# Kernel optimization log

Measured on AMD Instinct MI355X. Metric: run time of the kernel, lower is better.

## Reference

```python
import jax, jax.numpy as jnp
import numpy as np

V, B, C, H, W, D = 3, 2, 16, 128, 128, 32


def _skew(w):
    wx, wy, wz = w[..., 0], w[..., 1], w[..., 2]
    z = jnp.zeros_like(wx)
    return jnp.stack([
        jnp.stack([z, -wz, wy], -1),
        jnp.stack([wz, z, -wx], -1),
        jnp.stack([-wy, wx, z], -1)], -2)


def _rodrigues(w):
    th = jnp.linalg.norm(w, axis=-1, keepdims=True)
    n = w / (th + 1e-8)
    K = _skew(n)
    th = th[..., None]
    I = jnp.eye(3, dtype=w.dtype)
    return I + jnp.sin(th) * K + (1.0 - jnp.cos(th)) * (K @ K)


def setup_inputs() -> dict:
    key = jax.random.key(0)
    k1, k2, k3, k4 = jax.random.split(key, 4)
    features = jax.random.normal(k1, (V, B, C, H, W), jnp.float32)
    Kmat = jnp.array([[1.2 * W, 0.0, W / 2.0], [0.0, 1.2 * W, H / 2.0], [0.0, 0.0, 1.0]], jnp.float32)
    intrinsics = jnp.tile(Kmat, (V, B, 1, 1))
    rotvec = 0.05 * jax.random.normal(k2, (V, B, 3), jnp.float32)
    R = _rodrigues(rotvec)                                  # (V,B,3,3)
    t = 0.1 * jax.random.normal(k3, (V, B, 3), jnp.float32)
    top = jnp.concatenate([R, t[..., None]], -1)            # (V,B,3,4)
    bot = jnp.broadcast_to(jnp.array([0.0, 0.0, 0.0, 1.0], jnp.float32), (V, B, 1, 4))
    cam_to_world = jnp.concatenate([top, bot], -2)          # (V,B,4,4)
    depth_hypo = 1.0 + 9.0 * jax.random.uniform(k4, (B, D, H, W), jnp.float32)
    return {"features": features, "intrinsics": intrinsics,
            "cam_to_world": cam_to_world, "depth_hypo": depth_hypo}


def _grid_sample(img, grid):
    # img (B,C,H,W), grid (B,Hg,Wg,2) in [-1,1]; bilinear, zeros padding, align_corners=False
    Bb, Cc, Hh, Ww = img.shape
    gx = (grid[..., 0] + 1.0) * (Ww * 0.5) - 0.5
    gy = (grid[..., 1] + 1.0) * (Hh * 0.5) - 0.5
    x0f, y0f = jnp.floor(gx), jnp.floor(gy)
    fx, fy = gx - x0f, gy - y0f
    x0, y0 = x0f.astype(jnp.int32), y0f.astype(jnp.int32)

    def gather(xi, yi):
        valid = ((xi >= 0) & (xi < Ww) & (yi >= 0) & (yi < Hh)).astype(img.dtype)
        xc = jnp.clip(xi, 0, Ww - 1)
        yc = jnp.clip(yi, 0, Hh - 1)
        v = jax.vmap(lambda im, y, x: im[:, y, x])(img, yc, xc)  # (B,C,Hg,Wg)
        return v * valid[:, None]

    v00 = gather(x0, y0)
    v01 = gather(x0 + 1, y0)
    v10 = gather(x0, y0 + 1)
    v11 = gather(x0 + 1, y0 + 1)
    fx_, fy_ = fx[:, None], fy[:, None]
    return (v00 * (1 - fx_) * (1 - fy_) + v01 * fx_ * (1 - fy_)
            + v10 * (1 - fx_) * fy_ + v11 * fx_ * fy_)


def _unfold5(x):
    # x (B,K,H,W) -> (B,K,25,H,W); kernel 5, stride 1, pad 2; row-major kernel order (torch F.unfold)
    Hh, Ww = x.shape[-2], x.shape[-1]
    xp = jnp.pad(x, ((0, 0), (0, 0), (2, 2), (2, 2)))
    return jnp.stack([xp[..., i:i + Hh, j:j + Ww] for i in range(5) for j in range(5)], axis=2)


def _safe_norm(x, axis, keepdims=False):
    s = jnp.sum(x * x, axis=axis, keepdims=keepdims)
    z = s == 0
    return jnp.where(z, 0.0, jnp.sqrt(jnp.where(z, 1.0, s)))


def _homo_warp(src_f, depth_hypo, src_K, src_c2w, ref_K, ref_c2w):
    Bb, Cc, Hh, Ww = src_f.shape
    Dd = depth_hypo.shape[1]
    src_w2c = jnp.linalg.inv(src_c2w)
    ref_w2c = jnp.linalg.inv(ref_c2w)
    src_KK = src_w2c.at[:, :3, :3].set(src_K)
    ref_KK = ref_w2c.at[:, :3, :3].set(ref_K)
    proj = (src_KK @ src_w2c) @ jnp.linalg.inv(ref_KK @ ref_w2c)
    rot, trans = proj[:, :3, :3], proj[:, :3, 3:4]
    # NOTE: source uses arange(height) for both axes (square images assumed)
    ys, xs = jnp.meshgrid(jnp.arange(Hh, dtype=jnp.float32), jnp.arange(Hh, dtype=jnp.float32), indexing='ij')
    xyz = jnp.stack([xs.ravel(), ys.ravel(), jnp.ones(Hh * Ww, jnp.float32)], 0)  # (3,HW)
    rot_xyz = jnp.einsum('bij,jn->bin', rot, xyz)                                 # (B,3,HW)
    pts = rot_xyz[:, :, None, :] * depth_hypo.reshape(Bb, 1, Dd, -1) + trans[:, :, None, :]
    xy = pts[:, :2] / pts[:, 2:3]
    gx = xy[:, 0] / ((Ww - 1) / 2.0) - 1.0
    gy = xy[:, 1] / ((Hh - 1) / 2.0) - 1.0
    grid = jax.lax.stop_gradient(jnp.stack([gx, gy], -1).reshape(Bb, Dd * Hh, Ww, 2))
    return _grid_sample(src_f, grid).reshape(Bb, Cc, Dd, Hh, Ww)


def reference(features, intrinsics, cam_to_world, depth_hypo):
    Vv = features.shape[0]
    ref_f = features[0]
    warped = jnp.stack([
        _homo_warp(features[i], depth_hypo, intrinsics[i], cam_to_world[i],
                   intrinsics[0], cam_to_world[0]) for i in range(1, Vv)], 0)
    # faithful to in-place ref_volume.sub_: view k compares against ref - cumsum(warped[:k+1])
    diff = ref_f[None, :, :, None] - jnp.cumsum(warped, 0)        # (V-1,B,C,D,H,W)
    costs = _safe_norm(diff, axis=2)                              # (V-1,B,D,H,W)
    cost_volume = jnp.min(costs, axis=0)                          # (B,D,H,W)

    cnb = _unfold5(cost_volume)                                   # (B,D,25,H,W)
    dnb = _unfold5(depth_hypo)                                    # (B,D,25,H,W)
    w_depth = jax.nn.softmax(jnp.abs(dnb - dnb[:, :, 12:13]), axis=2)
    fnb = _unfold5(ref_f)                                         # (B,C,25,H,W)
    w_feat = _safe_norm(fnb - fnb[:, :, 12:13], axis=1, keepdims=True)  # (B,1,25,H,W)
    agg = jnp.sum(cnb * (w_depth * w_feat), axis=2)               # (B,D,H,W)

    prob = jax.nn.softmax(agg, axis=1)
    return jnp.sum(prob * depth_hypo, axis=1)                     # (B,H,W)
```

## Files before the change

kernel.cpp:

```cpp
#include <hip/hip_runtime.h>
#include <hip/hip_fp16.h>
#include <math.h>

#define Vn 3
#define Bn 2
#define Cn 16
#define Hn 128
#define Wn 128
#define Dn 32
#define HWn (Hn*Wn)
#define KD 4
#define PX 16


__device__ __forceinline__ void loadC8(float* r, const __half* p) {
    union { float4 f; __half2 h[4]; } u;
    u.f = *(const float4*)p;
    #pragma unroll
    for (int j = 0; j < 4; j++) {
        float2 a = __half22float2(u.h[j]);
        r[2*j] = a.x; r[2*j+1] = a.y;
    }
}

__global__ void transpose_kernel(const float* __restrict__ feat,
                                 __half* __restrict__ featH,
                                 const float* __restrict__ intr,
                                 const float* __restrict__ c2w,
                                 float* __restrict__ proj) {
    int idx = blockIdx.x * blockDim.x + threadIdx.x;
    if (idx < Vn * Bn * HWn) {
        int p  = idx % HWn;
        int vb = idx / HWn;
        const float* src = feat + (size_t)vb * Cn * HWn + p;
        union { float4 f[2]; __half h[16]; } u;
        #pragma unroll
        for (int c = 0; c < Cn; c++) u.h[c] = __float2half(src[(size_t)c * HWn]);
        __half* base = featH + (size_t)vb * 2 * HWn * 8;
        *(float4*)(base + (size_t)p * 8)              = u.f[0];
        *(float4*)(base + ((size_t)HWn + p) * 8)      = u.f[1];
    }

    if (blockIdx.x == 0 && threadIdx.x < (Vn - 1) * Bn) {
        int t  = threadIdx.x;
        int vi = t / Bn;
        int b  = t % Bn;
        int v  = vi + 1;

        const float* Ks = intr + (v * Bn + b) * 9;
        const float* Cs = c2w  + (v * Bn + b) * 16;
        const float* Kr = intr + (0 * Bn + b) * 9;
        const float* Cr = c2w  + (0 * Bn + b) * 16;

        float Ms[9], ms[3], Mr[9], mr[3];
        for (int which = 0; which < 2; which++) {
            const float* K = which ? Kr : Ks;
            const float* C = which ? Cr : Cs;
            float* M  = which ? Mr : Ms;
            float* mv = which ? mr : ms;
            float R[9], tt[3];
            for (int i = 0; i < 3; i++) {
                for (int j = 0; j < 3; j++) R[i*3+j] = C[i*4+j];
                tt[i] = C[i*4+3];
            }
            float tw[3];
            for (int i = 0; i < 3; i++)
                tw[i] = -(R[0*3+i]*tt[0] + R[1*3+i]*tt[1] + R[2*3+i]*tt[2]);
            for (int i = 0; i < 3; i++)
                for (int j = 0; j < 3; j++)
                    M[i*3+j] = K[i*3+0]*R[j*3+0] + K[i*3+1]*R[j*3+1] + K[i*3+2]*R[j*3+2];
            for (int i = 0; i < 3; i++)
                mv[i] = K[i*3+0]*tw[0] + K[i*3+1]*tw[1] + K[i*3+2]*tw[2] + tw[i];
        }

        float a = Mr[0], bb = Mr[1], c = Mr[2];
        float d = Mr[3], e  = Mr[4], f = Mr[5];
        float g = Mr[6], h  = Mr[7], i2 = Mr[8];
        float A_ = (e*i2 - f*h), B_ = (f*g - d*i2), C_ = (d*h - e*g);
        float det = a*A_ + bb*B_ + c*C_;
        float id = 1.0f / det;
        float inv[9];
        inv[0] = A_*id;            inv[1] = (c*h - bb*i2)*id;  inv[2] = (bb*f - c*e)*id;
        inv[3] = B_*id;            inv[4] = (a*i2 - c*g)*id;   inv[5] = (c*d - a*f)*id;
        inv[6] = C_*id;            inv[7] = (bb*g - a*h)*id;   inv[8] = (a*e - bb*d)*id;

        float rot[9], trans[3];
        for (int r = 0; r < 3; r++)
            for (int cc = 0; cc < 3; cc++)
                rot[r*3+cc] = Ms[r*3+0]*inv[0*3+cc] + Ms[r*3+1]*inv[1*3+cc] + Ms[r*3+2]*inv[2*3+cc];
        for (int r = 0; r < 3; r++)
            trans[r] = ms[r] - (rot[r*3+0]*mr[0] + rot[r*3+1]*mr[1] + rot[r*3+2]*mr[2]);

        float* o = proj + t * 12;
        for (int k = 0; k < 9; k++) o[k] = rot[k];
        for (int k = 0; k < 3; k++) o[9+k] = trans[k];
    }
}

__global__ void __launch_bounds__(256)
cost_kernel(const __half* __restrict__ featH,
            const float* __restrict__ depth,
            const float* __restrict__ proj,
            float* __restrict__ cv) {
    int idx = blockIdx.x * blockDim.x + threadIdx.x;
    if (idx >= Bn * (Dn/KD) * HWn) return;
    int x  = idx % Wn;
    int y  = (idx / Wn) % Hn;
    int dg = (idx / HWn) % (Dn/KD);
    int b  = idx / ((Dn/KD) * HWn);

    float dep[KD];
    #pragma unroll
    for (int i = 0; i < KD; i++)
        dep[i] = depth[(size_t)(b * Dn + dg*KD + i) * HWn + y * Wn + x];

    float ref[Cn];
    const __half* rbase = featH + (size_t)b * 2 * HWn * 8;
    loadC8(ref,     rbase + (size_t)(y * Wn + x) * 8);
    loadC8(ref + 8, rbase + ((size_t)HWn + y * Wn + x) * 8);

    const float fxp = (float)x, fyp = (float)y;

    float rxv[2], ryv[2], rzv[2], txv[2], tyv[2], tzv[2];
    #pragma unroll
    for (int vi = 0; vi < Vn - 1; vi++) {
        const float* P = proj + (vi * Bn + b) * 12;
        rxv[vi] = P[0]*fxp + P[1]*fyp + P[2];
        ryv[vi] = P[3]*fxp + P[4]*fyp + P[5];
        rzv[vi] = P[6]*fxp + P[7]*fyp + P[8];
        txv[vi] = P[9]; tyv[vi] = P[10]; tzv[vi] = P[11];
    }
    const __half* sfv[2] = {
        featH + (size_t)(1 * Bn + b) * 2 * HWn * 8,
        featH + (size_t)(2 * Bn + b) * 2 * HWn * 8
    };

    #pragma unroll
    for (int i = 0; i < KD; i++) {
        float cum[Cn];
        #pragma unroll
        for (int c = 0; c < Cn; c++) cum[c] = 0.0f;
        float smin = 3.402823e38f;

        #pragma unroll
        for (int vi = 0; vi < Vn - 1; vi++) {
            float px = rxv[vi] * dep[i] + txv[vi];
            float py = ryv[vi] * dep[i] + tyv[vi];
            float pz = rzv[vi] * dep[i] + tzv[vi];
            float inz = 1.0f / pz;
            float sx = px * inz * ((float)Wn / (float)(Wn - 1)) - 0.5f;
            float sy = py * inz * ((float)Hn / (float)(Hn - 1)) - 0.5f;

            float x0f = floorf(sx), y0f = floorf(sy);
            float fx = sx - x0f, fy = sy - y0f;
            int x0 = (int)x0f, y0 = (int)y0f;
            int x1 = x0 + 1, y1 = y0 + 1;
            bool vx0 = (x0 >= 0) && (x0 < Wn);
            bool vx1 = (x1 >= 0) && (x1 < Wn);
            bool vy0 = (y0 >= 0) && (y0 < Hn);
            bool vy1 = (y1 >= 0) && (y1 < Hn);
            int xc0 = min(max(x0, 0), Wn - 1), xc1 = min(max(x1, 0), Wn - 1);
            int yc0 = min(max(y0, 0), Hn - 1), yc1 = min(max(y1, 0), Hn - 1);
            float m00 = (vx0 && vy0) ? (1.0f - fx) * (1.0f - fy) : 0.0f;
            float m01 = (vx1 && vy0) ? fx * (1.0f - fy) : 0.0f;
            float m10 = (vx0 && vy1) ? (1.0f - fx) * fy : 0.0f;
            float m11 = (vx1 && vy1) ? fx * fy : 0.0f;

            const __half* sf = sfv[vi];
            size_t p00 = (size_t)(yc0 * Wn + xc0) * 8;
            size_t p01 = (size_t)(yc0 * Wn + xc1) * 8;
            size_t p10 = (size_t)(yc1 * Wn + xc0) * 8;
            size_t p11 = (size_t)(yc1 * Wn + xc1) * 8;
            const size_t hoff = (size_t)HWn * 8;

            float s = 0.0f;
            #pragma unroll
            for (int h = 0; h < 2; h++) {
                float t00[8], t01[8], t10[8], t11[8];
                loadC8(t00, sf + p00 + h * hoff);
                loadC8(t01, sf + p01 + h * hoff);
                loadC8(t10, sf + p10 + h * hoff);
                loadC8(t11, sf + p11 + h * hoff);
                #pragma unroll
                for (int j = 0; j < 8; j++) {
                    int c = h * 8 + j;
                    float val = m00 * t00[j] + m01 * t01[j] + m10 * t10[j] + m11 * t11[j];
                    cum[c] += val;
                    float df = ref[c] - cum[c];
                    s += df * df;
                }
            }
            smin = fminf(smin, s);
        }
        cv[(size_t)(b * Dn + dg*KD + i) * HWn + y * Wn + x] = sqrtf(smin);
    }
}

__global__ void __launch_bounds__(256)
aggfinal_kernel(const float* __restrict__ cv,
                const float* __restrict__ depth,
                const __half* __restrict__ featH,
                float* __restrict__ out) {
    __shared__ float sd[Dn][5][PX + 4];
    __shared__ float sc[Dn][5][PX + 4];
    __shared__ float4 sfeatv[5][PX + 4][2];
    __shared__ float swf[25][PX];
    __shared__ float sagg[Dn][PX];

    int bi = blockIdx.x;
    int xt = bi % (Wn / PX);
    int y  = (bi / (Wn / PX)) % Hn;
    int b  = bi / (Hn * (Wn / PX));
    int x0 = xt * PX;
    int tid = threadIdx.x;

    const int NS = Dn * 5 * (PX + 4);
    for (int s = tid; s < NS; s += 256) {
        int d  = s / (5 * (PX + 4));
        int r  = s % (5 * (PX + 4));
        int ny = r / (PX + 4);
        int nx = r % (PX + 4);
        int gy = y - 2 + ny;
        int gx = x0 - 2 + nx;
        float dv = 0.0f, cvv = 0.0f;
        if (gy >= 0 && gy < Hn && gx >= 0 && gx < Wn) {
            size_t off = (size_t)(b * Dn + d) * HWn + gy * Wn + gx;
            dv  = depth[off];
            cvv = cv[off];
        }
        sd[d][ny][nx] = dv;
        sc[d][ny][nx] = cvv;
    }
    const __half* fb = featH + (size_t)b * 2 * HWn * 8;
    for (int s = tid; s < 5 * (PX + 4); s += 256) {
        int ny = s / (PX + 4);
        int nx = s % (PX + 4);
        int gy = y - 2 + ny;
        int gx = x0 - 2 + nx;
        if (gy >= 0 && gy < Hn && gx >= 0 && gx < Wn) {
            sfeatv[ny][nx][0] = *(const float4*)(fb + (size_t)(gy * Wn + gx) * 8);
            sfeatv[ny][nx][1] = *(const float4*)(fb + ((size_t)HWn + gy * Wn + gx) * 8);
        } else {
            float4 z = make_float4(0.f, 0.f, 0.f, 0.f);
            sfeatv[ny][nx][0] = z;
            sfeatv[ny][nx][1] = z;
        }
    }
    __syncthreads();

    for (int s = tid; s < 25 * PX; s += 256) {
        int k   = s / PX;
        int xi2 = s % PX;
        const __half2* ctrp = (const __half2*)&sfeatv[2][xi2 + 2][0];
        const __half2* nbp  = (const __half2*)&sfeatv[k / 5][xi2 + (k % 5)][0];
        float acc = 0.0f;
        #pragma unroll
        for (int j = 0; j < 8; j++) {
            float2 a = __half22float2(nbp[j]);
            float2 c = __half22float2(ctrp[j]);
            float dx0 = a.x - c.x, dy0 = a.y - c.y;
            acc += dx0 * dx0 + dy0 * dy0;
        }
        swf[k][xi2] = sqrtf(acc);
    }
    __syncthreads();

    #pragma unroll
    for (int q = 0; q < 2; q++) {
        int task = tid + q * 256;
        int xi = task % PX;
        int d  = task / PX;

        float ctr = sd[d][2][xi + 2];
        float aarr[25];
        float mx = -3.402823e38f;
        #pragma unroll
        for (int k = 0; k < 25; k++) {
            float dn = sd[d][k / 5][xi + k % 5];
            aarr[k] = fabsf(dn - ctr);
            mx = fmaxf(mx, aarr[k]);
        }
        float den = 0.0f, num = 0.0f;
        #pragma unroll
        for (int k = 0; k < 25; k++) {
            float e = __expf(aarr[k] - mx);
            den += e;
            num += sc[d][k / 5][xi + k % 5] * e * swf[k][xi];
        }
        sagg[d][xi] = num / den;
    }
    __syncthreads();

    if (tid < PX) {
        int p = tid;
        float m = -3.402823e38f;
        #pragma unroll
        for (int dd = 0; dd < Dn; dd++)
            m = fmaxf(m, sagg[dd][p]);
        float dn2 = 0.0f, nm2 = 0.0f;
        #pragma unroll
        for (int dd = 0; dd < Dn; dd++) {
            float e = __expf(sagg[dd][p] - m);
            dn2 += e;
            nm2 += e * sd[dd][2][p + 2];
        }
        out[(size_t)(b * Hn + y) * Wn + x0 + p] = nm2 / dn2;
    }
}

extern "C" void kernel_launch(void* const* d_in, const int* in_sizes, int n_in,
                              void* d_out, int out_size, void* d_ws, size_t ws_size,
                              hipStream_t stream) {
    const float* feat  = (const float*)d_in[0];
    const float* intr  = (const float*)d_in[1];
    const float* c2w   = (const float*)d_in[2];
    const float* depth = (const float*)d_in[3];
    float* out = (float*)d_out;

    float* ws    = (float*)d_ws;
    float* proj  = ws;
    __half* featH = (__half*)(ws + 64);
    float* cv    = ws + 64 + (Vn * Bn * HWn * Cn) / 2;

    int n_tr = Vn * Bn * HWn;
    transpose_kernel<<<(n_tr + 255) / 256, 256, 0, stream>>>(feat, featH, intr, c2w, proj);

    int n_cost = Bn * (Dn / KD) * HWn;
    cost_kernel<<<(n_cost + 255) / 256, 256, 0, stream>>>(featH, depth, proj, cv);

    int n_blk = Bn * Hn * (Wn / PX);
    aggfinal_kernel<<<n_blk, 256, 0, stream>>>(cv, depth, featH, out);
}
```

Measured before the change: 113.8 us.

## Map one thread per depth hypothesis in cost kernel with depth-fastest indexing

The cost kernel now assigns one thread per (b, pixel, depth) with depth as the fastest-varying index, replacing the scheme where each thread handled four depths for one pixel. This gives 8x more threads and fewer registers per thread, and neighbouring lanes share a pixel, so the reference feature loads and projected sample locations stay close together. The trade-offs are uncoalesced depth reads and cost-volume writes (stride HW between lanes), plus recomputing the projection setup for every depth.

After: 114.0 us. No clear change (+0.1%).

```diff
diff --git a/kernel.cpp b/kernel.cpp
--- a/kernel.cpp
+++ b/kernel.cpp
@@ -9,7 +9,6 @@
 #define Wn 128
 #define Dn 32
 #define HWn (Hn*Wn)
-#define KD 4
 #define PX 16
 
 
@@ -37,8 +36,8 @@
         #pragma unroll
         for (int c = 0; c < Cn; c++) u.h[c] = __float2half(src[(size_t)c * HWn]);
         __half* base = featH + (size_t)vb * 2 * HWn * 8;
-        *(float4*)(base + (size_t)p * 8)              = u.f[0];
-        *(float4*)(base + ((size_t)HWn + p) * 8)      = u.f[1];
+        *(float4*)(base + (size_t)p * 8)         = u.f[0];
+        *(float4*)(base + ((size_t)HWn + p) * 8) = u.f[1];
     }
 
     if (blockIdx.x == 0 && threadIdx.x < (Vn - 1) * Bn) {
@@ -103,97 +102,83 @@
             const float* __restrict__ proj,
             float* __restrict__ cv) {
     int idx = blockIdx.x * blockDim.x + threadIdx.x;
-    if (idx >= Bn * (Dn/KD) * HWn) return;
-    int x  = idx % Wn;
-    int y  = (idx / Wn) % Hn;
-    int dg = (idx / HWn) % (Dn/KD);
-    int b  = idx / ((Dn/KD) * HWn);
-
-    float dep[KD];
-    #pragma unroll
-    for (int i = 0; i < KD; i++)
-        dep[i] = depth[(size_t)(b * Dn + dg*KD + i) * HWn + y * Wn + x];
+    if (idx >= Bn * HWn * Dn) return;
+    int d = idx & (Dn - 1);
+    int x = (idx >> 5)  & (Wn - 1);
+    int y = (idx >> 12) & (Hn - 1);
+    int b = idx >> 19;
+
+    const int pix = y * Wn + x;
+    float dep = depth[(size_t)(b * Dn + d) * HWn + pix];
 
     float ref[Cn];
     const __half* rbase = featH + (size_t)b * 2 * HWn * 8;
-    loadC8(ref,     rbase + (size_t)(y * Wn + x) * 8);
-    loadC8(ref + 8, rbase + ((size_t)HWn + y * Wn + x) * 8);
+    loadC8(ref,     rbase + (size_t)pix * 8);
+    loadC8(ref + 8, rbase + ((size_t)HWn + pix) * 8);
 
     const float fxp = (float)x, fyp = (float)y;
 
-    float rxv[2], ryv[2], rzv[2], txv[2], tyv[2], tzv[2];
+    float cum[Cn];
+    #pragma unroll
+    for (int c = 0; c < Cn; c++) cum[c] = 0.0f;
+    float smin = 3.402823e38f;
+
     #pragma unroll
     for (int vi = 0; vi < Vn - 1; vi++) {
         const float* P = proj + (vi * Bn + b) * 12;
-        rxv[vi] = P[0]*fxp + P[1]*fyp + P[2];
-        ryv[vi] = P[3]*fxp + P[4]*fyp + P[5];
-        rzv[vi] = P[6]*fxp + P[7]*fyp + P[8];
-        txv[vi] = P[9]; tyv[vi] = P[10]; tzv[vi] = P[11];
-    }
-    const __half* sfv[2] = {
-        featH + (size_t)(1 * Bn + b) * 2 * HWn * 8,
-        featH + (size_t)(2 * Bn + b) * 2 * HWn * 8
-    };
-
-    #pragma unroll
-    for (int i = 0; i < KD; i++) {
-        float cum[Cn];
-        #pragma unroll
-        for (int c = 0; c < Cn; c++) cum[c] = 0.0f;
-        float smin = 3.402823e38f;
-
-        #pragma unroll
-        for (int vi = 0; vi < Vn - 1; vi++) {
-            float px = rxv[vi] * dep[i] + txv[vi];
-            float py = ryv[vi] * dep[i] + tyv[vi];
-            float pz = rzv[vi] * dep[i] + tzv[vi];
-            float inz = 1.0f / pz;
-            float sx = px * inz * ((float)Wn / (float)(Wn - 1)) - 0.5f;
-            float sy = py * inz * ((float)Hn / (float)(Hn - 1)) - 0.5f;
-
-            float x0f = floorf(sx), y0f = floorf(sy);
-            float fx = sx - x0f, fy = sy - y0f;
-            int x0 = (int)x0f, y0 = (int)y0f;
-            int x1 = x0 + 1, y1 = y0 + 1;
-            bool vx0 = (x0 >= 0) && (x0 < Wn);
-            bool vx1 = (x1 >= 0) && (x1 < Wn);
-            bool vy0 = (y0 >= 0) && (y0 < Hn);
-            bool vy1 = (y1 >= 0) && (y1 < Hn);
-            int xc0 = min(max(x0, 0), Wn - 1), xc1 = min(max(x1, 0), Wn - 1);
-            int yc0 = min(max(y0, 0), Hn - 1), yc1 = min(max(y1, 0), Hn - 1);
-            float m00 = (vx0 && vy0) ? (1.0f - fx) * (1.0f - fy) : 0.0f;
-            float m01 = (vx1 && vy0) ? fx * (1.0f - fy) : 0.0f;
-            float m10 = (vx0 && vy1) ? (1.0f - fx) * fy : 0.0f;
-            float m11 = (vx1 && vy1) ? fx * fy : 0.0f;
-
-            const __half* sf = sfv[vi];
-            size_t p00 = (size_t)(yc0 * Wn + xc0) * 8;
-            size_t p01 = (size_t)(yc0 * Wn + xc1) * 8;
-            size_t p10 = (size_t)(yc1 * Wn + xc0) * 8;
-            size_t p11 = (size_t)(yc1 * Wn + xc1) * 8;
-            const size_t hoff = (size_t)HWn * 8;
-
-            float s = 0.0f;
+        float rx = P[0]*fxp + P[1]*fyp + P[2];
+        float ry = P[3]*fxp + P[4]*fyp + P[5];
+        float rz = P[6]*fxp + P[7]*fyp + P[8];
+
+        float px = rx * dep + P[9];
+        float py = ry * dep + P[10];
+        float pz = rz * dep + P[11];
+        float inz = 1.0f / pz;
+        float sx = px * inz * ((float)Wn / (float)(Wn - 1)) - 0.5f;
+        float sy = py * inz * ((float)Hn / (float)(Hn - 1)) - 0.5f;
+
+        float x0f = floorf(sx), y0f = floorf(sy);
+        float fx = sx - x0f, fy = sy - y0f;
+        int x0 = (int)x0f, y0 = (int)y0f;
+        int x1 = x0 + 1, y1 = y0 + 1;
+        bool vx0 = (x0 >= 0) && (x0 < Wn);
+        bool vx1 = (x1 >= 0) && (x1 < Wn);
+        bool vy0 = (y0 >= 0) && (y0 < Hn);
+        bool vy1 = (y1 >= 0) && (y1 < Hn);
+        int xc0 = min(max(x0, 0), Wn - 1), xc1 = min(max(x1, 0), Wn - 1);
+        int yc0 = min(max(y0, 0), Hn - 1), yc1 = min(max(y1, 0), Hn - 1);
+        float m00 = (vx0 && vy0) ? (1.0f - fx) * (1.0f - fy) : 0.0f;
+        float m01 = (vx1 && vy0) ? fx * (1.0f - fy) : 0.0f;
+        float m10 = (vx0 && vy1) ? (1.0f - fx) * fy : 0.0f;
+        float m11 = (vx1 && vy1) ? fx * fy : 0.0f;
+
+        const __half* sf = featH + (size_t)((vi + 1) * Bn + b) * 2 * HWn * 8;
+        int p00 = (yc0 * Wn + xc0) * 8;
+        int p01 = (yc0 * Wn + xc1) * 8;
+        int p10 = (yc1 * Wn + xc0) * 8;
+        int p11 = (yc1 * Wn + xc1) * 8;
+        const int hoff = HWn * 8;
+
+        float s = 0.0f;
+        #pragma unroll
+        for (int h = 0; h < 2; h++) {
+            float t00[8], t01[8], t10[8], t11[8];
+            loadC8(t00, sf + p00 + h * hoff);
+            loadC8(t01, sf + p01 + h * hoff);
+            loadC8(t10, sf + p10 + h * hoff);
+            loadC8(t11, sf + p11 + h * hoff);
             #pragma unroll
-            for (int h = 0; h < 2; h++) {
-                float t00[8], t01[8], t10[8], t11[8];
-                loadC8(t00, sf + p00 + h * hoff);
-                loadC8(t01, sf + p01 + h * hoff);
-                loadC8(t10, sf + p10 + h * hoff);
-                loadC8(t11, sf + p11 + h * hoff);
-                #pragma unroll
-                for (int j = 0; j < 8; j++) {
-                    int c = h * 8 + j;
-                    float val = m00 * t00[j] + m01 * t01[j] + m10 * t10[j] + m11 * t11[j];
-                    cum[c] += val;
-                    float df = ref[c] - cum[c];
-                    s += df * df;
-                }
+            for (int j = 0; j < 8; j++) {
+                int c = h * 8 + j;
+                float val = m00 * t00[j] + m01 * t01[j] + m10 * t10[j] + m11 * t11[j];
+                cum[c] += val;
+                float df = ref[c] - cum[c];
+                s += df * df;
             }
-            smin = fminf(smin, s);
-        }
-        cv[(size_t)(b * Dn + dg*KD + i) * HWn + y * Wn + x] = sqrtf(smin);
-    }
+        }
+        smin = fminf(smin, s);
+    }
+    cv[(size_t)(b * Dn + d) * HWn + pix] = sqrtf(smin);
 }
 
 __global__ void __launch_bounds__(256)
@@ -325,7 +310,7 @@
     int n_tr = Vn * Bn * HWn;
     transpose_kernel<<<(n_tr + 255) / 256, 256, 0, stream>>>(feat, featH, intr, c2w, proj);
 
-    int n_cost = Bn * (Dn / KD) * HWn;
+    int n_cost = Bn * HWn * Dn;
     cost_kernel<<<(n_cost + 255) / 256, 256, 0, stream>>>(featH, depth, proj, cv);
 
     int n_blk = Bn * Hn * (Wn / PX);
```
